# Optimization experiments

Hardware: AMD Instinct MI355X
Metric: run time of the kernel (lower is better)

The kernel has to match this reference:

```python
import jax, jax.numpy as jnp
import numpy as np

T_STEPS = 64   # number of actions (T-1 in the torch code)
BATCH = 512
STATE = 256
ACTION = 64
BELIEF = 1024
HIDDEN = 1024
EMB = 1024
MIN_STD = 0.1


def setup_inputs() -> dict:
    key = jax.random.key(0)
    ks = jax.random.split(key, 16)
    def w(k, shape):
        return jax.random.normal(k, shape, jnp.float32) * 0.02
    return {
        "s_0": jax.random.normal(ks[0], (BATCH, STATE), jnp.float32),
        "A": jax.random.normal(ks[1], (T_STEPS, BATCH, ACTION), jnp.float32),
        "b_0": jax.random.normal(ks[2], (BATCH, BELIEF), jnp.float32),
        "O": jax.random.normal(ks[3], (T_STEPS, BATCH, EMB), jnp.float32),
        "M": jnp.ones((T_STEPS, BATCH, 1), jnp.float32),
        "noise_pri": jax.random.normal(ks[4], (T_STEPS, BATCH, STATE), jnp.float32),
        "noise_pos": jax.random.normal(ks[5], (T_STEPS, BATCH, STATE), jnp.float32),
        # learned parameters (torch nn.Linear convention: y = x @ W.T + b)
        "W_sa": w(ks[6], (BELIEF, STATE + ACTION)), "b_sa": jnp.zeros((BELIEF,), jnp.float32),
        "W_ih": w(ks[7], (3 * BELIEF, BELIEF)), "b_ih": jnp.zeros((3 * BELIEF,), jnp.float32),
        "W_hh": w(ks[8], (3 * BELIEF, BELIEF)), "b_hh": jnp.zeros((3 * BELIEF,), jnp.float32),
        "W_bpri": w(ks[9], (HIDDEN, BELIEF)), "b_bpri": jnp.zeros((HIDDEN,), jnp.float32),
        "W_spri": w(ks[10], (2 * STATE, HIDDEN)), "b_spri": jnp.zeros((2 * STATE,), jnp.float32),
        "W_bpos": w(ks[11], (HIDDEN, BELIEF + EMB)), "b_bpos": jnp.zeros((HIDDEN,), jnp.float32),
        "W_spos": w(ks[12], (2 * STATE, HIDDEN)), "b_spos": jnp.zeros((2 * STATE,), jnp.float32),
    }


def reference(s_0, A, b_0, O, M, noise_pri, noise_pos,
              W_sa, b_sa, W_ih, b_ih, W_hh, b_hh,
              W_bpri, b_bpri, W_spri, b_spri,
              W_bpos, b_bpos, W_spos, b_spos):
    act = jax.nn.relu  # cfg.activation_function = 'relu'

    def gru_cell(x, h):
        # torch GRUCell gate order: r, z, n
        gi = x @ W_ih.T + b_ih      # [B, 3*BELIEF]
        gh = h @ W_hh.T + b_hh
        i_r, i_z, i_n = jnp.split(gi, 3, axis=1)
        h_r, h_z, h_n = jnp.split(gh, 3, axis=1)
        r = jax.nn.sigmoid(i_r + h_r)
        z = jax.nn.sigmoid(i_z + h_z)
        n = jnp.tanh(i_n + r * h_n)
        return (1.0 - z) * n + z * h

    def step(carry, xs):
        b, s = carry  # belief [B,BELIEF], posterior state [B,STATE]
        a_t, o_t, m_t, eps_p, eps_q = xs
        s_in = s * m_t  # non-terminal mask
        x = act(jnp.concatenate([s_in, a_t], axis=1) @ W_sa.T + b_sa)
        b_new = gru_cell(x, b)
        # prior
        pri = act(b_new @ W_bpri.T + b_bpri) @ W_spri.T + b_spri
        mu_p, hp = jnp.split(pri, 2, axis=1)
        std_p = jax.nn.softplus(hp) + MIN_STD
        s_p = mu_p + std_p * eps_p
        # posterior (uses current observation embedding)
        pos = act(jnp.concatenate([b_new, o_t], axis=1) @ W_bpos.T + b_bpos) @ W_spos.T + b_spos
        mu_q, hq = jnp.split(pos, 2, axis=1)
        std_q = jax.nn.softplus(hq) + MIN_STD
        s_q = mu_q + std_q * eps_q
        return (b_new, s_q), (b_new, s_p, mu_p, std_p, s_q, mu_q, std_q)

    (_, _), ys = jax.lax.scan(step, (b_0, s_0), (A, O, M, noise_pri, noise_pos))
    B_out, S_pri, MU_pri, STD_pri, S_pos, MU_pos, STD_pos = ys
    return B_out, S_pri, MU_pri, STD_pri, S_pos, MU_pos, STD_pos
```

## Files before the change

kernel.cpp:

```cpp
#include <hip/hip_runtime.h>
#include <hip/hip_bf16.h>
#include <math.h>

typedef short bf16x8 __attribute__((ext_vector_type(8)));
typedef float f32x4 __attribute__((ext_vector_type(4)));
typedef unsigned short u16;

#define NT 64
#define NB 512
#define NS 256
#define NA 64
#define NBEL 1024

#define OUT_B      0
#define OUT_SPRI   33554432
#define OUT_MUPRI  41943040
#define OUT_STDPRI 50331648
#define OUT_SPOS   58720256
#define OUT_MUPOS  67108864
#define OUT_STDPOS 75497472

__device__ __forceinline__ f32x4 mfma16(bf16x8 a, bf16x8 b, f32x4 c) {
  return __builtin_amdgcn_mfma_f32_16x16x32_bf16(a, b, c, 0, 0, 0);
}

__device__ __forceinline__ u16 f2bf(float f) {
  union { float f; unsigned u; } v; v.f = f;
  return (u16)((v.u + 0x7FFFu + ((v.u >> 16) & 1u)) >> 16);
}

__device__ __forceinline__ bf16x8 ld8bf(const u16* p) { return *(const bf16x8*)p; }

__device__ __forceinline__ bf16x8 cvt8(const float* p) {
  const float4 lo = *(const float4*)p;
  const float4 hi = *(const float4*)(p + 4);
  bf16x8 v;
  v[0] = (short)f2bf(lo.x); v[1] = (short)f2bf(lo.y);
  v[2] = (short)f2bf(lo.z); v[3] = (short)f2bf(lo.w);
  v[4] = (short)f2bf(hi.x); v[5] = (short)f2bf(hi.y);
  v[6] = (short)f2bf(hi.z); v[7] = (short)f2bf(hi.w);
  return v;
}

__device__ __forceinline__ float sigm(float x) { return 1.f / (1.f + __expf(-x)); }
__device__ __forceinline__ float softplus_(float x) {
  if (x > 20.f) return x;
  return log1pf(__expf(x));
}

#define ZACC(acc) { acc[0][0] = (f32x4){0.f,0.f,0.f,0.f}; acc[0][1] = (f32x4){0.f,0.f,0.f,0.f}; \
                    acc[1][0] = (f32x4){0.f,0.f,0.f,0.f}; acc[1][1] = (f32x4){0.f,0.f,0.f,0.f}; }

#define Q4(acc, a0v, a1v, b0v, b1v) \
  acc[0][0] = mfma16(a0v, b0v, acc[0][0]); \
  acc[0][1] = mfma16(a0v, b1v, acc[0][1]); \
  acc[1][0] = mfma16(a1v, b0v, acc[1][0]); \
  acc[1][1] = mfma16(a1v, b1v, acc[1][1]);

__device__ __forceinline__ void red_write(float* L, f32x4 (&acc)[2][2], int l) {
  const int base = l * 16;
#pragma unroll
  for (int i = 0; i < 2; ++i)
#pragma unroll
    for (int j = 0; j < 2; ++j)
#pragma unroll
      for (int q = 0; q < 4; ++q)
        L[base + (i * 2 + j) * 4 + q] = acc[i][j][q];
}
__device__ __forceinline__ void red_add(const float* L, f32x4 (&acc)[2][2], int l) {
  const int base = l * 16;
#pragma unroll
  for (int i = 0; i < 2; ++i)
#pragma unroll
    for (int j = 0; j < 2; ++j)
#pragma unroll
      for (int q = 0; q < 4; ++q)
        acc[i][j][q] += L[base + (i * 2 + j) * 4 + q];
}

__global__ __launch_bounds__(256) void cvt_weights_k(
    const float* __restrict__ wsa, const float* __restrict__ wih,
    const float* __restrict__ whh, const float* __restrict__ wbpri,
    const float* __restrict__ wspri, const float* __restrict__ wbpos,
    const float* __restrict__ wspos, u16* __restrict__ dst) {
  const int S0 = 327680;
  const int S1 = S0 + 3145728;
  const int S2 = S1 + 3145728;
  const int S3 = S2 + 1048576;
  const int S4 = S3 + 524288;
  const int S5 = S4 + 2097152;
  const int S6 = S5 + 524288;
  for (int i = blockIdx.x * blockDim.x + threadIdx.x; i < S6;
       i += gridDim.x * blockDim.x) {
    float v;
    if (i < S0) v = wsa[i];
    else if (i < S1) v = wih[i - S0];
    else if (i < S2) v = whh[i - S1];
    else if (i < S3) v = wbpri[i - S2];
    else if (i < S4) v = wspri[i - S3];
    else if (i < S5) v = wbpos[i - S4];
    else v = wspos[i - S5];
    dst[i] = f2bf(v);
  }
}

__global__ __launch_bounds__(256) void init_carry_k(
    const float* __restrict__ s0, const float* __restrict__ b0,
    const float* __restrict__ Mptr, u16* __restrict__ smask,
    u16* __restrict__ bbf0, float* __restrict__ hf) {
  for (int i = blockIdx.x * blockDim.x + threadIdx.x; i < NB * NBEL;
       i += gridDim.x * blockDim.x) {
    float b = b0[i];
    bbf0[i] = f2bf(b);
    hf[i] = b;
    if (i < NB * NS) {
      int row = i >> 8;
      smask[i] = f2bf(s0[i] * Mptr[row]);
    }
  }
}

__global__ __launch_bounds__(512, 2) void kA(
    const u16* __restrict__ smask, const float* __restrict__ Af,
    const u16* __restrict__ wsa, const float* __restrict__ bsa,
    u16* __restrict__ xbf, const float* __restrict__ Of,
    const u16* __restrict__ wbpos, float* __restrict__ hbO, int t) {
  __shared__ float lred[4][1024];
  const int l = threadIdx.x & 63, r16 = l & 15, kq = l >> 4;
  const int wid8 = threadIdx.x >> 6;
  const int wid = wid8 & 3, kh = wid8 >> 2;
  if (blockIdx.x < 128) {
    const int g = blockIdx.x, bm = g >> 4, bn = g & 15;
    const int row0 = bm * 64 + (wid >> 1) * 32;
    const int col0 = bn * 64 + (wid & 1) * 32;
    f32x4 acc[2][2]; ZACC(acc);
    const u16* A0 = smask + (row0 + r16) * NS + kq * 8;
    const u16* A1 = A0 + 16 * NS;
    const u16* B0 = wsa + (size_t)(col0 + r16) * 320 + kq * 8;
    const u16* B1 = B0 + 16 * 320;
    if (kh == 0) {
#pragma unroll
      for (int k = 0; k < 160; k += 32) {
        bf16x8 a0 = ld8bf(A0 + k), a1 = ld8bf(A1 + k);
        bf16x8 b0 = ld8bf(B0 + k), b1 = ld8bf(B1 + k);
        Q4(acc, a0, a1, b0, b1);
      }
    } else {
#pragma unroll
      for (int k = 160; k < 256; k += 32) {
        bf16x8 a0 = ld8bf(A0 + k), a1 = ld8bf(A1 + k);
        bf16x8 b0 = ld8bf(B0 + k), b1 = ld8bf(B1 + k);
        Q4(acc, a0, a1, b0, b1);
      }
      const float* F0 = Af + (size_t)t * (NB * NA) + (row0 + r16) * NA + kq * 8;
      const float* F1 = F0 + 16 * NA;
      const u16* C0 = wsa + (size_t)(col0 + r16) * 320 + 256 + kq * 8;
      const u16* C1 = C0 + 16 * 320;
#pragma unroll
      for (int k = 0; k < 64; k += 32) {
        bf16x8 a0 = cvt8(F0 + k), a1 = cvt8(F1 + k);
        bf16x8 b0 = ld8bf(C0 + k), b1 = ld8bf(C1 + k);
        Q4(acc, a0, a1, b0, b1);
      }
      red_write(lred[wid], acc, l);
    }
    __syncthreads();
    if (kh == 0) {
      red_add(lred[wid], acc, l);
#pragma unroll
      for (int i = 0; i < 2; ++i)
#pragma unroll
        for (int j = 0; j < 2; ++j)
#pragma unroll
          for (int q = 0; q < 4; ++q) {
            const int row = row0 + i * 16 + kq * 4 + q;
            const int col = col0 + j * 16 + r16;
            xbf[row * NBEL + col] = f2bf(fmaxf(acc[i][j][q] + bsa[col], 0.f));
          }
    }
  } else {
    const int g = blockIdx.x - 128, bm = g >> 4, bn = g & 15;
    const int row0 = bm * 64 + (wid >> 1) * 32;
    const int col0 = bn * 64 + (wid & 1) * 32;
    f32x4 acc[2][2]; ZACC(acc);
    const float* F0 = Of + (size_t)t * (NB * NBEL) + (row0 + r16) * NBEL + kh * 512 + kq * 8;
    const float* F1 = F0 + 16 * NBEL;
    const u16* B0 = wbpos + (size_t)(col0 + r16) * 2048 + 1024 + kh * 512 + kq * 8;
    const u16* B1 = B0 + 16 * 2048;
#pragma unroll 4
    for (int k = 0; k < 512; k += 32) {
      bf16x8 a0 = cvt8(F0 + k), a1 = cvt8(F1 + k);
      bf16x8 b0 = ld8bf(B0 + k), b1 = ld8bf(B1 + k);
      Q4(acc, a0, a1, b0, b1);
    }
    if (kh == 1) red_write(lred[wid], acc, l);
    __syncthreads();
    if (kh == 0) {
      red_add(lred[wid], acc, l);
#pragma unroll
      for (int i = 0; i < 2; ++i)
#pragma unroll
        for (int j = 0; j < 2; ++j)
#pragma unroll
          for (int q = 0; q < 4; ++q) {
            const int row = row0 + i * 16 + kq * 4 + q;
            const int col = col0 + j * 16 + r16;
            hbO[row * NBEL + col] = acc[i][j][q];
          }
    }
  }
}

__global__ __launch_bounds__(512, 2) void kB(
    const u16* __restrict__ xbf, const u16* __restrict__ bprev,
    const u16* __restrict__ wih, const u16* __restrict__ whh,
    const float* __restrict__ bih, const float* __restrict__ bhh,
    float* __restrict__ hf, u16* __restrict__ bcur, float* __restrict__ out,
    const u16* __restrict__ wbpri, const float* __restrict__ bbpri,
    u16* __restrict__ hpri, int t) {
  __shared__ float lred[4][3][1024];
  const int l = threadIdx.x & 63, r16 = l & 15, kq = l >> 4;
  const int wid8 = threadIdx.x >> 6;
  const int wid = wid8 & 3, kh = wid8 >> 2;
  if (blockIdx.x < 128) {
    if (t >= NT) return;
    const int g = blockIdx.x, bm = g >> 4, bn = g & 15;
    const int row0 = bm * 64 + (wid >> 1) * 32;
    const int col0 = bn * 64 + (wid & 1) * 32;
    f32x4 ar[2][2], az[2][2], an[2][2];
    ZACC(ar); ZACC(az); ZACC(an);
    const u16* Asrc = (kh == 0) ? xbf : bprev;
    const u16* W = (kh == 0) ? wih : whh;
    const u16* A0 = Asrc + (row0 + r16) * NBEL + kq * 8;
    const u16* A1 = A0 + 16 * NBEL;
    const u16* Br0 = W + (size_t)(col0 + r16) * NBEL + kq * 8;
    const u16* Br1 = Br0 + 16 * NBEL;
    const u16* Bz0 = W + (size_t)(col0 + 1024 + r16) * NBEL + kq * 8;
    const u16* Bz1 = Bz0 + 16 * NBEL;
    const u16* Bn0 = W + (size_t)(col0 + 2048 + r16) * NBEL + kq * 8;
    const u16* Bn1 = Bn0 + 16 * NBEL;
#pragma unroll 4
    for (int k = 0; k < NBEL; k += 32) {
      bf16x8 a0 = ld8bf(A0 + k), a1 = ld8bf(A1 + k);
      bf16x8 b0 = ld8bf(Br0 + k), b1 = ld8bf(Br1 + k);
      Q4(ar, a0, a1, b0, b1);
      bf16x8 c0 = ld8bf(Bz0 + k), c1 = ld8bf(Bz1 + k);
      Q4(az, a0, a1, c0, c1);
      bf16x8 d0 = ld8bf(Bn0 + k), d1 = ld8bf(Bn1 + k);
      Q4(an, a0, a1, d0, d1);
    }
    if (kh == 1) {
      red_write(lred[wid][0], ar, l);
      red_write(lred[wid][1], az, l);
      red_write(lred[wid][2], an, l);
    }
    __syncthreads();
    if (kh == 0) {
      const int base = l * 16;
#pragma unroll
      for (int i = 0; i < 2; ++i)
#pragma unroll
        for (int j = 0; j < 2; ++j)
#pragma unroll
          for (int q = 0; q < 4; ++q) {
            const int row = row0 + i * 16 + kq * 4 + q;
            const int c = col0 + j * 16 + r16;
            const int li = base + (i * 2 + j) * 4 + q;
            const float r = sigm(ar[i][j][q] + bih[c] + lred[wid][0][li] + bhh[c]);
            const float z = sigm(az[i][j][q] + bih[c + 1024] + lred[wid][1][li] + bhh[c + 1024]);
            const float n = tanhf(an[i][j][q] + bih[c + 2048] +
                                  r * (lred[wid][2][li] + bhh[c + 2048]));
            const float h = hf[row * NBEL + c];
            const float bnew = (1.f - z) * n + z * h;
            hf[row * NBEL + c] = bnew;
            bcur[row * NBEL + c] = f2bf(bnew);
            out[OUT_B + (size_t)t * (NB * NBEL) + row * NBEL + c] = bnew;
          }
    }
  } else {
    if (t < 1) return;
    const int g = blockIdx.x - 128, bm = g >> 4, bn = g & 15;
    const int row0 = bm * 64 + (wid >> 1) * 32;
    const int col0 = bn * 64 + (wid & 1) * 32;
    f32x4 acc[2][2]; ZACC(acc);
    const u16* A0 = bprev + (row0 + r16) * NBEL + kh * 512 + kq * 8;
    const u16* A1 = A0 + 16 * NBEL;
    const u16* B0 = wbpri + (size_t)(col0 + r16) * NBEL + kh * 512 + kq * 8;
    const u16* B1 = B0 + 16 * NBEL;
#pragma unroll 4
    for (int k = 0; k < 512; k += 32) {
      bf16x8 a0 = ld8bf(A0 + k), a1 = ld8bf(A1 + k);
      bf16x8 b0 = ld8bf(B0 + k), b1 = ld8bf(B1 + k);
      Q4(acc, a0, a1, b0, b1);
    }
    if (kh == 1) red_write(lred[wid][0], acc, l);
    __syncthreads();
    if (kh == 0) {
      red_add(lred[wid][0], acc, l);
#pragma unroll
      for (int i = 0; i < 2; ++i)
#pragma unroll
        for (int j = 0; j < 2; ++j)
#pragma unroll
          for (int q = 0; q < 4; ++q) {
            const int row = row0 + i * 16 + kq * 4 + q;
            const int col = col0 + j * 16 + r16;
            hpri[row * NBEL + col] = f2bf(fmaxf(acc[i][j][q] + bbpri[col], 0.f));
          }
    }
  }
}

__global__ __launch_bounds__(512, 2) void kC(
    const u16* __restrict__ bcur, const u16* __restrict__ wbpos,
    const float* __restrict__ bbpos, const float* __restrict__ hbO,
    u16* __restrict__ hbbf,
    const u16* __restrict__ hpri, const u16* __restrict__ wspri,
    const float* __restrict__ bspri, const float* __restrict__ npri,
    float* __restrict__ out, int t) {
  __shared__ float lred[4][2][1024];
  const int l = threadIdx.x & 63, r16 = l & 15, kq = l >> 4;
  const int wid8 = threadIdx.x >> 6;
  const int wid = wid8 & 3, kh = wid8 >> 2;
  if (blockIdx.x < 128) {
    if (t >= NT) return;
    const int g = blockIdx.x, bm = g >> 4, bn = g & 15;
    const int row0 = bm * 64 + (wid >> 1) * 32;
    const int col0 = bn * 64 + (wid & 1) * 32;
    f32x4 acc[2][2]; ZACC(acc);
    const u16* A0 = bcur + (row0 + r16) * NBEL + kh * 512 + kq * 8;
    const u16* A1 = A0 + 16 * NBEL;
    const u16* B0 = wbpos + (size_t)(col0 + r16) * 2048 + kh * 512 + kq * 8;
    const u16* B1 = B0 + 16 * 2048;
#pragma unroll 4
    for (int k = 0; k < 512; k += 32) {
      bf16x8 a0 = ld8bf(A0 + k), a1 = ld8bf(A1 + k);
      bf16x8 b0 = ld8bf(B0 + k), b1 = ld8bf(B1 + k);
      Q4(acc, a0, a1, b0, b1);
    }
    if (kh == 1) red_write(lred[wid][0], acc, l);
    __syncthreads();
    if (kh == 0) {
      red_add(lred[wid][0], acc, l);
#pragma unroll
      for (int i = 0; i < 2; ++i)
#pragma unroll
        for (int j = 0; j < 2; ++j)
#pragma unroll
          for (int q = 0; q < 4; ++q) {
            const int row = row0 + i * 16 + kq * 4 + q;
            const int col = col0 + j * 16 + r16;
            const float v = acc[i][j][q] + hbO[row * NBEL + col] + bbpos[col];
            hbbf[row * NBEL + col] = f2bf(fmaxf(v, 0.f));
          }
    }
  } else {
    if (t < 1) return;
    const int g = blockIdx.x - 128, bm = g >> 2, bn = g & 3;
    const int row0 = bm * 64 + (wid >> 1) * 32;
    const int c0 = bn * 64 + (wid & 1) * 32;
    f32x4 am[2][2], ah[2][2];
    ZACC(am); ZACC(ah);
    const u16* A0 = hpri + (row0 + r16) * NBEL + kh * 512 + kq * 8;
    const u16* A1 = A0 + 16 * NBEL;
    const u16* Bm0 = wspri + (size_t)(c0 + r16) * NBEL + kh * 512 + kq * 8;
    const u16* Bm1 = Bm0 + 16 * NBEL;
    const u16* Bh0 = wspri + (size_t)(c0 + 256 + r16) * NBEL + kh * 512 + kq * 8;
    const u16* Bh1 = Bh0 + 16 * NBEL;
#pragma unroll 4
    for (int k = 0; k < 512; k += 32) {
      bf16x8 a0 = ld8bf(A0 + k), a1 = ld8bf(A1 + k);
      bf16x8 m0 = ld8bf(Bm0 + k), m1 = ld8bf(Bm1 + k);
      Q4(am, a0, a1, m0, m1);
      bf16x8 h0 = ld8bf(Bh0 + k), h1 = ld8bf(Bh1 + k);
      Q4(ah, a0, a1, h0, h1);
    }
    if (kh == 1) {
      red_write(lred[wid][0], am, l);
      red_write(lred[wid][1], ah, l);
    }
    __syncthreads();
    if (kh == 0) {
      red_add(lred[wid][0], am, l);
      red_add(lred[wid][1], ah, l);
      const int tt = t - 1;
#pragma unroll
      for (int i = 0; i < 2; ++i)
#pragma unroll
        for (int j = 0; j < 2; ++j)
#pragma unroll
          for (int q = 0; q < 4; ++q) {
            const int row = row0 + i * 16 + kq * 4 + q;
            const int c = c0 + j * 16 + r16;
            const size_t idx = (size_t)tt * (NB * NS) + row * NS + c;
            const float mu = am[i][j][q] + bspri[c];
            const float hp = ah[i][j][q] + bspri[c + 256];
            const float sd = softplus_(hp) + 0.1f;
            out[OUT_SPRI + idx] = mu + sd * npri[idx];
            out[OUT_MUPRI + idx] = mu;
            out[OUT_STDPRI + idx] = sd;
          }
    }
  }
}

__global__ __launch_bounds__(512, 2) void kD(
    const u16* __restrict__ hbbf, const u16* __restrict__ wspos,
    const float* __restrict__ bspos, const float* __restrict__ npos,
    const float* __restrict__ Mptr, float* __restrict__ out,
    u16* __restrict__ smask, int t) {
  __shared__ float lred[4][2][1024];
  const int l = threadIdx.x & 63, r16 = l & 15, kq = l >> 4;
  const int wid8 = threadIdx.x >> 6;
  const int wid = wid8 & 3, kh = wid8 >> 2;
  const int g = blockIdx.x, bm = g >> 2, bn = g & 3;
  const int row0 = bm * 64 + (wid >> 1) * 32;
  const int c0 = bn * 64 + (wid & 1) * 32;
  f32x4 am[2][2], ah[2][2];
  ZACC(am); ZACC(ah);
  const u16* A0 = hbbf + (row0 + r16) * NBEL + kh * 512 + kq * 8;
  const u16* A1 = A0 + 16 * NBEL;
  const u16* Bm0 = wspos + (size_t)(c0 + r16) * NBEL + kh * 512 + kq * 8;
  const u16* Bm1 = Bm0 + 16 * NBEL;
  const u16* Bh0 = wspos + (size_t)(c0 + 256 + r16) * NBEL + kh * 512 + kq * 8;
  const u16* Bh1 = Bh0 + 16 * NBEL;
#pragma unroll 4
  for (int k = 0; k < 512; k += 32) {
    bf16x8 a0 = ld8bf(A0 + k), a1 = ld8bf(A1 + k);
    bf16x8 m0 = ld8bf(Bm0 + k), m1 = ld8bf(Bm1 + k);
    Q4(am, a0, a1, m0, m1);
    bf16x8 h0 = ld8bf(Bh0 + k), h1 = ld8bf(Bh1 + k);
    Q4(ah, a0, a1, h0, h1);
  }
  if (kh == 1) {
    red_write(lred[wid][0], am, l);
    red_write(lred[wid][1], ah, l);
  }
  __syncthreads();
  if (kh == 0) {
    red_add(lred[wid][0], am, l);
    red_add(lred[wid][1], ah, l);
#pragma unroll
    for (int i = 0; i < 2; ++i)
#pragma unroll
      for (int j = 0; j < 2; ++j)
#pragma unroll
        for (int q = 0; q < 4; ++q) {
          const int row = row0 + i * 16 + kq * 4 + q;
          const int c = c0 + j * 16 + r16;
          const float mu = am[i][j][q] + bspos[c];
          const float hq = ah[i][j][q] + bspos[c + 256];
          const float sd = softplus_(hq) + 0.1f;
          const size_t idx = (size_t)t * (NB * NS) + row * NS + c;
          const float sq = mu + sd * npos[idx];
          out[OUT_SPOS + idx] = sq;
          out[OUT_MUPOS + idx] = mu;
          out[OUT_STDPOS + idx] = sd;
          const float mn = (t < NT - 1) ? Mptr[(t + 1) * NB + row] : 1.f;
          smask[row * NS + c] = f2bf(sq * mn);
        }
  }
}

extern "C" void kernel_launch(void* const* d_in, const int* in_sizes, int n_in,
                              void* d_out, int out_size, void* d_ws, size_t ws_size,
                              hipStream_t stream) {
  const float* s0 = (const float*)d_in[0];
  const float* Af = (const float*)d_in[1];
  const float* b0 = (const float*)d_in[2];
  const float* Of = (const float*)d_in[3];
  const float* Mp = (const float*)d_in[4];
  const float* npri = (const float*)d_in[5];
  const float* npos = (const float*)d_in[6];
  const float* Wsa = (const float*)d_in[7];
  const float* bsa = (const float*)d_in[8];
  const float* Wih = (const float*)d_in[9];
  const float* bih = (const float*)d_in[10];
  const float* Whh = (const float*)d_in[11];
  const float* bhh = (const float*)d_in[12];
  const float* Wbpri = (const float*)d_in[13];
  const float* bbpri = (const float*)d_in[14];
  const float* Wspri = (const float*)d_in[15];
  const float* bspri = (const float*)d_in[16];
  const float* Wbpos = (const float*)d_in[17];
  const float* bbpos = (const float*)d_in[18];
  const float* Wspos = (const float*)d_in[19];
  const float* bspos = (const float*)d_in[20];

  float* out = (float*)d_out;
  char* ws = (char*)d_ws;
  u16* wbase   = (u16*)ws;
  u16* wsa_b   = wbase;
  u16* wih_b   = wbase + 327680;
  u16* whh_b   = wbase + 3473408;
  u16* wbpri_b = wbase + 6619136;
  u16* wspri_b = wbase + 7667712;
  u16* wbpos_b = wbase + 8192000;
  u16* wspos_b = wbase + 10289152;
  u16*   smask = (u16*)  (ws + 21626880);
  u16*   bbf0  = (u16*)  (ws + 21889024);
  u16*   bbf1  = (u16*)  (ws + 22937600);
  float* hf    = (float*)(ws + 23986176);
  u16*   xbf   = (u16*)  (ws + 26083328);
  float* hbO   = (float*)(ws + 27131904);
  u16*   hbbf  = (u16*)  (ws + 29229056);
  u16*   hpri  = (u16*)  (ws + 30277632);

  cvt_weights_k<<<2048, 256, 0, stream>>>(Wsa, Wih, Whh, Wbpri, Wspri, Wbpos,
                                          Wspos, wbase);
  init_carry_k<<<2048, 256, 0, stream>>>(s0, b0, Mp, smask, bbf0, hf);

  for (int t = 0; t < NT; ++t) {
    const u16* bprev = (t & 1) ? bbf1 : bbf0;
    u16* bcur = (t & 1) ? bbf0 : bbf1;
    kA<<<256, 512, 0, stream>>>(smask, Af, wsa_b, bsa, xbf, Of, wbpos_b, hbO, t);
    kB<<<256, 512, 0, stream>>>(xbf, bprev, wih_b, whh_b, bih, bhh, hf, bcur,
                                out, wbpri_b, bbpri, hpri, t);
    kC<<<160, 512, 0, stream>>>(bcur, wbpos_b, bbpos, hbO, hbbf,
                                hpri, wspri_b, bspri, npri, out, t);
    kD<<<32, 512, 0, stream>>>(hbbf, wspos_b, bspos, npos, Mp, out, smask, t);
  }
  {
    const int t = NT;
    const u16* bprev = (t & 1) ? bbf1 : bbf0;
    u16* bcur = (t & 1) ? bbf0 : bbf1;
    kB<<<256, 512, 0, stream>>>(xbf, bprev, wih_b, whh_b, bih, bhh, hf, bcur,
                                out, wbpri_b, bbpri, hpri, t);
    kC<<<160, 512, 0, stream>>>(bcur, wbpos_b, bbpos, hbO, hbbf,
                                hpri, wspri_b, bspri, npri, out, t);
  }
}
```

Before: 10.06 ms.

## Hoist GRU hidden matmul and obs projection into previous step's kernel, fuse x into GRU

Moves the h@W_hh GEMM and the next step's observation projection into the kC kernel, which runs as soon as the new belief exists, so they overlap the prior/posterior head work. The s/a input GEMM is recomputed per block inside the GRU kernel and kept in swizzled LDS, which removes the separate kA launch and the xbf round trip through global memory. This drops one launch per step and shortens the serial chain. In exchange each GRU block does redundant W_sa work, there is an extra fp32 gh buffer, and the kernels are larger with a 128KB LDS footprint.

```diff
diff --git a/kernel.cpp b/kernel.cpp
--- a/kernel.cpp
+++ b/kernel.cpp
@@ -76,6 +76,10 @@
 #pragma unroll
       for (int q = 0; q < 4; ++q)
         acc[i][j][q] += L[base + (i * 2 + j) * 4 + q];
+}
+
+__device__ __forceinline__ int xls_off(int row, int col) {
+  return ((row * NBEL + col) * 2) ^ ((row & 7) << 4);
 }
 
 __global__ __launch_bounds__(256) void cvt_weights_k(
@@ -120,128 +124,162 @@
   }
 }
 
-__global__ __launch_bounds__(512, 2) void kA(
-    const u16* __restrict__ smask, const float* __restrict__ Af,
-    const u16* __restrict__ wsa, const float* __restrict__ bsa,
-    u16* __restrict__ xbf, const float* __restrict__ Of,
-    const u16* __restrict__ wbpos, float* __restrict__ hbO, int t) {
-  __shared__ float lred[4][1024];
+
+__device__ __forceinline__ void dev_gh128(
+    int g, int wid8, int r16, int kq,
+    const u16* __restrict__ bsrc, const u16* __restrict__ whh,
+    const float* __restrict__ bhh, float* __restrict__ gh) {
+  const int bm = g / 24, bn = g % 24;
+  const int row0 = bm * 64 + (wid8 >> 2) * 32;
+  const int col0 = bn * 128 + (wid8 & 3) * 32;
+  f32x4 acc[2][2]; ZACC(acc);
+  const u16* A0 = bsrc + (row0 + r16) * NBEL + kq * 8;
+  const u16* A1 = A0 + 16 * NBEL;
+  const u16* B0 = whh + (size_t)(col0 + r16) * NBEL + kq * 8;
+  const u16* B1 = B0 + 16 * NBEL;
+#pragma unroll 4
+  for (int k = 0; k < NBEL; k += 32) {
+    bf16x8 a0 = ld8bf(A0 + k), a1 = ld8bf(A1 + k);
+    bf16x8 b0 = ld8bf(B0 + k), b1 = ld8bf(B1 + k);
+    Q4(acc, a0, a1, b0, b1);
+  }
+#pragma unroll
+  for (int i = 0; i < 2; ++i)
+#pragma unroll
+    for (int j = 0; j < 2; ++j)
+#pragma unroll
+      for (int q = 0; q < 4; ++q) {
+        const int row = row0 + i * 16 + kq * 4 + q;
+        const int col = col0 + j * 16 + r16;
+        gh[row * 3072 + col] = acc[i][j][q] + bhh[col];
+      }
+}
+
+__device__ __forceinline__ void dev_hbO(
+    int g, int wid, int kh, int r16, int kq, int l, int tt,
+    const float* __restrict__ Of, const u16* __restrict__ wbpos,
+    float* __restrict__ hbO, float* lred) {
+  const int bm = g >> 4, bn = g & 15;
+  const int row0 = bm * 64 + (wid >> 1) * 32;
+  const int col0 = bn * 64 + (wid & 1) * 32;
+  f32x4 acc[2][2]; ZACC(acc);
+  const float* F0 = Of + (size_t)tt * (NB * NBEL) + (row0 + r16) * NBEL + kh * 512 + kq * 8;
+  const float* F1 = F0 + 16 * NBEL;
+  const u16* B0 = wbpos + (size_t)(col0 + r16) * 2048 + 1024 + kh * 512 + kq * 8;
+  const u16* B1 = B0 + 16 * 2048;
+#pragma unroll 4
+  for (int k = 0; k < 512; k += 32) {
+    bf16x8 a0 = cvt8(F0 + k), a1 = cvt8(F1 + k);
+    bf16x8 b0 = ld8bf(B0 + k), b1 = ld8bf(B1 + k);
+    Q4(acc, a0, a1, b0, b1);
+  }
+  if (kh == 1) red_write(lred, acc, l);
+  __syncthreads();
+  if (kh == 0) {
+    red_add(lred, acc, l);
+#pragma unroll
+    for (int i = 0; i < 2; ++i)
+#pragma unroll
+      for (int j = 0; j < 2; ++j)
+#pragma unroll
+        for (int q = 0; q < 4; ++q) {
+          const int row = row0 + i * 16 + kq * 4 + q;
+          const int col = col0 + j * 16 + r16;
+          hbO[row * NBEL + col] = acc[i][j][q];
+        }
+  }
+}
+
+__global__ __launch_bounds__(512, 2) void kPre(
+    const u16* __restrict__ bbf0, const u16* __restrict__ whh,
+    const float* __restrict__ bhh, float* __restrict__ gh,
+    const float* __restrict__ Of, const u16* __restrict__ wbpos,
+    float* __restrict__ hbO0) {
+  __shared__ float lred[4][3][1024];
   const int l = threadIdx.x & 63, r16 = l & 15, kq = l >> 4;
   const int wid8 = threadIdx.x >> 6;
   const int wid = wid8 & 3, kh = wid8 >> 2;
-  if (blockIdx.x < 128) {
-    const int g = blockIdx.x, bm = g >> 4, bn = g & 15;
-    const int row0 = bm * 64 + (wid >> 1) * 32;
-    const int col0 = bn * 64 + (wid & 1) * 32;
-    f32x4 acc[2][2]; ZACC(acc);
-    const u16* A0 = smask + (row0 + r16) * NS + kq * 8;
-    const u16* A1 = A0 + 16 * NS;
-    const u16* B0 = wsa + (size_t)(col0 + r16) * 320 + kq * 8;
-    const u16* B1 = B0 + 16 * 320;
-    if (kh == 0) {
-#pragma unroll
-      for (int k = 0; k < 160; k += 32) {
-        bf16x8 a0 = ld8bf(A0 + k), a1 = ld8bf(A1 + k);
-        bf16x8 b0 = ld8bf(B0 + k), b1 = ld8bf(B1 + k);
-        Q4(acc, a0, a1, b0, b1);
-      }
-    } else {
-#pragma unroll
-      for (int k = 160; k < 256; k += 32) {
-        bf16x8 a0 = ld8bf(A0 + k), a1 = ld8bf(A1 + k);
-        bf16x8 b0 = ld8bf(B0 + k), b1 = ld8bf(B1 + k);
-        Q4(acc, a0, a1, b0, b1);
-      }
-      const float* F0 = Af + (size_t)t * (NB * NA) + (row0 + r16) * NA + kq * 8;
-      const float* F1 = F0 + 16 * NA;
-      const u16* C0 = wsa + (size_t)(col0 + r16) * 320 + 256 + kq * 8;
-      const u16* C1 = C0 + 16 * 320;
-#pragma unroll
-      for (int k = 0; k < 64; k += 32) {
-        bf16x8 a0 = cvt8(F0 + k), a1 = cvt8(F1 + k);
-        bf16x8 b0 = ld8bf(C0 + k), b1 = ld8bf(C1 + k);
-        Q4(acc, a0, a1, b0, b1);
-      }
-      red_write(lred[wid], acc, l);
-    }
-    __syncthreads();
-    if (kh == 0) {
-      red_add(lred[wid], acc, l);
-#pragma unroll
-      for (int i = 0; i < 2; ++i)
-#pragma unroll
-        for (int j = 0; j < 2; ++j)
-#pragma unroll
-          for (int q = 0; q < 4; ++q) {
-            const int row = row0 + i * 16 + kq * 4 + q;
-            const int col = col0 + j * 16 + r16;
-            xbf[row * NBEL + col] = f2bf(fmaxf(acc[i][j][q] + bsa[col], 0.f));
-          }
-    }
+  if (blockIdx.x < 192) {
+    dev_gh128(blockIdx.x, wid8, r16, kq, bbf0, whh, bhh, gh);
   } else {
-    const int g = blockIdx.x - 128, bm = g >> 4, bn = g & 15;
-    const int row0 = bm * 64 + (wid >> 1) * 32;
-    const int col0 = bn * 64 + (wid & 1) * 32;
-    f32x4 acc[2][2]; ZACC(acc);
-    const float* F0 = Of + (size_t)t * (NB * NBEL) + (row0 + r16) * NBEL + kh * 512 + kq * 8;
-    const float* F1 = F0 + 16 * NBEL;
-    const u16* B0 = wbpos + (size_t)(col0 + r16) * 2048 + 1024 + kh * 512 + kq * 8;
-    const u16* B1 = B0 + 16 * 2048;
-#pragma unroll 4
-    for (int k = 0; k < 512; k += 32) {
-      bf16x8 a0 = cvt8(F0 + k), a1 = cvt8(F1 + k);
-      bf16x8 b0 = ld8bf(B0 + k), b1 = ld8bf(B1 + k);
-      Q4(acc, a0, a1, b0, b1);
-    }
-    if (kh == 1) red_write(lred[wid], acc, l);
-    __syncthreads();
-    if (kh == 0) {
-      red_add(lred[wid], acc, l);
-#pragma unroll
-      for (int i = 0; i < 2; ++i)
-#pragma unroll
-        for (int j = 0; j < 2; ++j)
-#pragma unroll
-          for (int q = 0; q < 4; ++q) {
-            const int row = row0 + i * 16 + kq * 4 + q;
-            const int col = col0 + j * 16 + r16;
-            hbO[row * NBEL + col] = acc[i][j][q];
-          }
-    }
-  }
-}
-
-__global__ __launch_bounds__(512, 2) void kB(
-    const u16* __restrict__ xbf, const u16* __restrict__ bprev,
-    const u16* __restrict__ wih, const u16* __restrict__ whh,
-    const float* __restrict__ bih, const float* __restrict__ bhh,
-    float* __restrict__ hf, u16* __restrict__ bcur, float* __restrict__ out,
+    dev_hbO(blockIdx.x - 192, wid, kh, r16, kq, l, 0, Of, wbpos, hbO0,
+            &lred[wid][0][0]);
+  }
+}
+
+__global__ __launch_bounds__(512, 2) void kB2(
+    const u16* __restrict__ smask, const float* __restrict__ Af,
+    const u16* __restrict__ wsa, const float* __restrict__ bsa,
+    const u16* __restrict__ wih, const float* __restrict__ bih,
+    const float* __restrict__ gh, float* __restrict__ hf,
+    const u16* __restrict__ bprev, u16* __restrict__ bcur,
+    float* __restrict__ out,
     const u16* __restrict__ wbpri, const float* __restrict__ bbpri,
     u16* __restrict__ hpri, int t) {
-  __shared__ float lred[4][3][1024];
+  __shared__ __align__(16) char smem[131072];
   const int l = threadIdx.x & 63, r16 = l & 15, kq = l >> 4;
   const int wid8 = threadIdx.x >> 6;
   const int wid = wid8 & 3, kh = wid8 >> 2;
   if (blockIdx.x < 128) {
     if (t >= NT) return;
     const int g = blockIdx.x, bm = g >> 4, bn = g & 15;
-    const int row0 = bm * 64 + (wid >> 1) * 32;
+    for (int task = wid8; task < 16; task += 8) {
+      const int lr0 = (task & 1) * 32;
+      const int c0t = (task >> 1) * 128;
+      const int grow = bm * 64 + lr0;
+      for (int jt = 0; jt < 4; ++jt) {
+        const int col = c0t + jt * 32;
+        f32x4 acc[2][2]; ZACC(acc);
+        const u16* A0 = smask + (grow + r16) * NS + kq * 8;
+        const u16* A1 = A0 + 16 * NS;
+        const u16* B0 = wsa + (size_t)(col + r16) * 320 + kq * 8;
+        const u16* B1 = B0 + 16 * 320;
+#pragma unroll
+        for (int k = 0; k < 256; k += 32) {
+          bf16x8 a0 = ld8bf(A0 + k), a1 = ld8bf(A1 + k);
+          bf16x8 b0 = ld8bf(B0 + k), b1 = ld8bf(B1 + k);
+          Q4(acc, a0, a1, b0, b1);
+        }
+        const float* F0 = Af + (size_t)t * (NB * NA) + (grow + r16) * NA + kq * 8;
+        const float* F1 = F0 + 16 * NA;
+        const u16* C0 = wsa + (size_t)(col + r16) * 320 + 256 + kq * 8;
+        const u16* C1 = C0 + 16 * 320;
+#pragma unroll
+        for (int k = 0; k < 64; k += 32) {
+          bf16x8 a0 = cvt8(F0 + k), a1 = cvt8(F1 + k);
+          bf16x8 b0 = ld8bf(C0 + k), b1 = ld8bf(C1 + k);
+          Q4(acc, a0, a1, b0, b1);
+        }
+#pragma unroll
+        for (int i = 0; i < 2; ++i)
+#pragma unroll
+          for (int j = 0; j < 2; ++j)
+#pragma unroll
+            for (int q = 0; q < 4; ++q) {
+              const int lr = lr0 + i * 16 + kq * 4 + q;
+              const int c = col + j * 16 + r16;
+              const u16 v = f2bf(fmaxf(acc[i][j][q] + bsa[c], 0.f));
+              *(u16*)(smem + xls_off(lr, c)) = v;
+            }
+      }
+    }
+    __syncthreads();
+    const int lrow0 = (wid >> 1) * 32;
+    const int grow0 = bm * 64 + lrow0;
     const int col0 = bn * 64 + (wid & 1) * 32;
     f32x4 ar[2][2], az[2][2], an[2][2];
     ZACC(ar); ZACC(az); ZACC(an);
-    const u16* Asrc = (kh == 0) ? xbf : bprev;
-    const u16* W = (kh == 0) ? wih : whh;
-    const u16* A0 = Asrc + (row0 + r16) * NBEL + kq * 8;
-    const u16* A1 = A0 + 16 * NBEL;
-    const u16* Br0 = W + (size_t)(col0 + r16) * NBEL + kq * 8;
+    const u16* Br0 = wih + (size_t)(col0 + r16) * NBEL + kh * 512 + kq * 8;
     const u16* Br1 = Br0 + 16 * NBEL;
-    const u16* Bz0 = W + (size_t)(col0 + 1024 + r16) * NBEL + kq * 8;
+    const u16* Bz0 = wih + (size_t)(col0 + 1024 + r16) * NBEL + kh * 512 + kq * 8;
     const u16* Bz1 = Bz0 + 16 * NBEL;
-    const u16* Bn0 = W + (size_t)(col0 + 2048 + r16) * NBEL + kq * 8;
+    const u16* Bn0 = wih + (size_t)(col0 + 2048 + r16) * NBEL + kh * 512 + kq * 8;
     const u16* Bn1 = Bn0 + 16 * NBEL;
 #pragma unroll 4
-    for (int k = 0; k < NBEL; k += 32) {
-      bf16x8 a0 = ld8bf(A0 + k), a1 = ld8bf(A1 + k);
+    for (int k = 0; k < 512; k += 32) {
+      const int ks = kh * 512 + k + kq * 8;
+      bf16x8 a0 = *(const bf16x8*)(smem + xls_off(lrow0 + r16, ks));
+      bf16x8 a1 = *(const bf16x8*)(smem + xls_off(lrow0 + 16 + r16, ks));
       bf16x8 b0 = ld8bf(Br0 + k), b1 = ld8bf(Br1 + k);
       Q4(ar, a0, a1, b0, b1);
       bf16x8 c0 = ld8bf(Bz0 + k), c1 = ld8bf(Bz1 + k);
@@ -249,10 +287,12 @@
       bf16x8 d0 = ld8bf(Bn0 + k), d1 = ld8bf(Bn1 + k);
       Q4(an, a0, a1, d0, d1);
     }
+    __syncthreads();
+    float (*lred)[3][1024] = (float (*)[3][1024])smem;
     if (kh == 1) {
-      red_write(lred[wid][0], ar, l);
-      red_write(lred[wid][1], az, l);
-      red_write(lred[wid][2], an, l);
+      red_write(&lred[wid][0][0], ar, l);
+      red_write(&lred[wid][1][0], az, l);
+      red_write(&lred[wid][2][0], an, l);
     }
     __syncthreads();
     if (kh == 0) {
@@ -263,13 +303,14 @@
         for (int j = 0; j < 2; ++j)
 #pragma unroll
           for (int q = 0; q < 4; ++q) {
-            const int row = row0 + i * 16 + kq * 4 + q;
+            const int row = grow0 + i * 16 + kq * 4 + q;
             const int c = col0 + j * 16 + r16;
             const int li = base + (i * 2 + j) * 4 + q;
-            const float r = sigm(ar[i][j][q] + bih[c] + lred[wid][0][li] + bhh[c]);
-            const float z = sigm(az[i][j][q] + bih[c + 1024] + lred[wid][1][li] + bhh[c + 1024]);
-            const float n = tanhf(an[i][j][q] + bih[c + 2048] +
-                                  r * (lred[wid][2][li] + bhh[c + 2048]));
+            const float* ghrow = gh + row * 3072;
+            const float r = sigm(ar[i][j][q] + lred[wid][0][li] + bih[c] + ghrow[c]);
+            const float z = sigm(az[i][j][q] + lred[wid][1][li] + bih[c + 1024] + ghrow[c + 1024]);
+            const float n = tanhf(an[i][j][q] + lred[wid][2][li] + bih[c + 2048] +
+                                  r * ghrow[c + 2048]);
             const float h = hf[row * NBEL + c];
             const float bnew = (1.f - z) * n + z * h;
             hf[row * NBEL + c] = bnew;
@@ -279,6 +320,7 @@
     }
   } else {
     if (t < 1) return;
+    float (*lred)[3][1024] = (float (*)[3][1024])smem;
     const int g = blockIdx.x - 128, bm = g >> 4, bn = g & 15;
     const int row0 = bm * 64 + (wid >> 1) * 32;
     const int col0 = bn * 64 + (wid & 1) * 32;
@@ -293,10 +335,10 @@
       bf16x8 b0 = ld8bf(B0 + k), b1 = ld8bf(B1 + k);
       Q4(acc, a0, a1, b0, b1);
     }
-    if (kh == 1) red_write(lred[wid][0], acc, l);
+    if (kh == 1) red_write(&lred[wid][0][0], acc, l);
     __syncthreads();
     if (kh == 0) {
-      red_add(lred[wid][0], acc, l);
+      red_add(&lred[wid][0][0], acc, l);
 #pragma unroll
       for (int i = 0; i < 2; ++i)
 #pragma unroll
@@ -311,14 +353,17 @@
   }
 }
 
-__global__ __launch_bounds__(512, 2) void kC(
+__global__ __launch_bounds__(512, 2) void kC2(
     const u16* __restrict__ bcur, const u16* __restrict__ wbpos,
-    const float* __restrict__ bbpos, const float* __restrict__ hbO,
+    const float* __restrict__ bbpos, const float* __restrict__ hbOc,
     u16* __restrict__ hbbf,
+    const u16* __restrict__ whh, const float* __restrict__ bhh,
+    float* __restrict__ gh,
+    const float* __restrict__ Of, float* __restrict__ hbOn,
     const u16* __restrict__ hpri, const u16* __restrict__ wspri,
     const float* __restrict__ bspri, const float* __restrict__ npri,
     float* __restrict__ out, int t) {
-  __shared__ float lred[4][2][1024];
+  __shared__ float lred[4][3][1024];
   const int l = threadIdx.x & 63, r16 = l & 15, kq = l >> 4;
   const int wid8 = threadIdx.x >> 6;
   const int wid = wid8 & 3, kh = wid8 >> 2;
@@ -338,10 +383,10 @@
       bf16x8 b0 = ld8bf(B0 + k), b1 = ld8bf(B1 + k);
       Q4(acc, a0, a1, b0, b1);
     }
-    if (kh == 1) red_write(lred[wid][0], acc, l);
+    if (kh == 1) red_write(&lred[wid][0][0], acc, l);
     __syncthreads();
     if (kh == 0) {
-      red_add(lred[wid][0], acc, l);
+      red_add(&lred[wid][0][0], acc, l);
 #pragma unroll
       for (int i = 0; i < 2; ++i)
 #pragma unroll
@@ -350,13 +395,20 @@
           for (int q = 0; q < 4; ++q) {
             const int row = row0 + i * 16 + kq * 4 + q;
             const int col = col0 + j * 16 + r16;
-            const float v = acc[i][j][q] + hbO[row * NBEL + col] + bbpos[col];
+            const float v = acc[i][j][q] + hbOc[row * NBEL + col] + bbpos[col];
             hbbf[row * NBEL + col] = f2bf(fmaxf(v, 0.f));
           }
     }
+  } else if (blockIdx.x < 320) {
+    if (t + 1 >= NT) return;
+    dev_gh128(blockIdx.x - 128, wid8, r16, kq, bcur, whh, bhh, gh);
+  } else if (blockIdx.x < 448) {
+    if (t + 1 >= NT) return;
+    dev_hbO(blockIdx.x - 320, wid, kh, r16, kq, l, t + 1, Of, wbpos, hbOn,
+            &lred[wid][0][0]);
   } else {
     if (t < 1) return;
-    const int g = blockIdx.x - 128, bm = g >> 2, bn = g & 3;
+    const int g = blockIdx.x - 448, bm = g >> 2, bn = g & 3;
     const int row0 = bm * 64 + (wid >> 1) * 32;
     const int c0 = bn * 64 + (wid & 1) * 32;
     f32x4 am[2][2], ah[2][2];
@@ -376,13 +428,13 @@
       Q4(ah, a0, a1, h0, h1);
     }
     if (kh == 1) {
-      red_write(lred[wid][0], am, l);
-      red_write(lred[wid][1], ah, l);
+      red_write(&lred[wid][0][0], am, l);
+      red_write(&lred[wid][1][0], ah, l);
     }
     __syncthreads();
     if (kh == 0) {
-      red_add(lred[wid][0], am, l);
-      red_add(lred[wid][1], ah, l);
+      red_add(&lred[wid][0][0], am, l);
+      red_add(&lred[wid][1][0], ah, l);
       const int tt = t - 1;
 #pragma unroll
       for (int i = 0; i < 2; ++i)
@@ -433,13 +485,13 @@
     Q4(ah, a0, a1, h0, h1);
   }
   if (kh == 1) {
-    red_write(lred[wid][0], am, l);
-    red_write(lred[wid][1], ah, l);
+    red_write(&lred[wid][0][0], am, l);
+    red_write(&lred[wid][1][0], ah, l);
   }
   __syncthreads();
   if (kh == 0) {
-    red_add(lred[wid][0], am, l);
-    red_add(lred[wid][1], ah, l);
+    red_add(&lred[wid][0][0], am, l);
+    red_add(&lred[wid][1][0], ah, l);
 #pragma unroll
     for (int i = 0; i < 2; ++i)
 #pragma unroll
@@ -501,32 +553,39 @@
   u16*   bbf0  = (u16*)  (ws + 21889024);
   u16*   bbf1  = (u16*)  (ws + 22937600);
   float* hf    = (float*)(ws + 23986176);
-  u16*   xbf   = (u16*)  (ws + 26083328);
-  float* hbO   = (float*)(ws + 27131904);
-  u16*   hbbf  = (u16*)  (ws + 29229056);
-  u16*   hpri  = (u16*)  (ws + 30277632);
+  float* gh    = (float*)(ws + 26083328);
+  float* hbO0  = (float*)(ws + 32374784);
+  float* hbO1  = (float*)(ws + 34471936);
+  u16*   hbbf  = (u16*)  (ws + 36569088);
+  u16*   hpri  = (u16*)  (ws + 37617664);
 
   cvt_weights_k<<<2048, 256, 0, stream>>>(Wsa, Wih, Whh, Wbpri, Wspri, Wbpos,
                                           Wspos, wbase);
   init_carry_k<<<2048, 256, 0, stream>>>(s0, b0, Mp, smask, bbf0, hf);
+  kPre<<<320, 512, 0, stream>>>(bbf0, whh_b, bhh, gh, Of, wbpos_b, hbO0);
 
   for (int t = 0; t < NT; ++t) {
     const u16* bprev = (t & 1) ? bbf1 : bbf0;
     u16* bcur = (t & 1) ? bbf0 : bbf1;
-    kA<<<256, 512, 0, stream>>>(smask, Af, wsa_b, bsa, xbf, Of, wbpos_b, hbO, t);
-    kB<<<256, 512, 0, stream>>>(xbf, bprev, wih_b, whh_b, bih, bhh, hf, bcur,
-                                out, wbpri_b, bbpri, hpri, t);
-    kC<<<160, 512, 0, stream>>>(bcur, wbpos_b, bbpos, hbO, hbbf,
-                                hpri, wspri_b, bspri, npri, out, t);
+    float* hbOc = (t & 1) ? hbO1 : hbO0;
+    float* hbOn = (t & 1) ? hbO0 : hbO1;
+    kB2<<<256, 512, 0, stream>>>(smask, Af, wsa_b, bsa, wih_b, bih, gh, hf,
+                                 bprev, bcur, out, wbpri_b, bbpri, hpri, t);
+    kC2<<<480, 512, 0, stream>>>(bcur, wbpos_b, bbpos, hbOc, hbbf,
+                                 whh_b, bhh, gh, Of, hbOn,
+                                 hpri, wspri_b, bspri, npri, out, t);
     kD<<<32, 512, 0, stream>>>(hbbf, wspos_b, bspos, npos, Mp, out, smask, t);
   }
   {
     const int t = NT;
     const u16* bprev = (t & 1) ? bbf1 : bbf0;
     u16* bcur = (t & 1) ? bbf0 : bbf1;
-    kB<<<256, 512, 0, stream>>>(xbf, bprev, wih_b, whh_b, bih, bhh, hf, bcur,
-                                out, wbpri_b, bbpri, hpri, t);
-    kC<<<160, 512, 0, stream>>>(bcur, wbpos_b, bbpos, hbO, hbbf,
-                                hpri, wspri_b, bspri, npri, out, t);
-  }
-}
+    float* hbOc = (t & 1) ? hbO1 : hbO0;
+    float* hbOn = (t & 1) ? hbO0 : hbO1;
+    kB2<<<256, 512, 0, stream>>>(smask, Af, wsa_b, bsa, wih_b, bih, gh, hf,
+                                 bprev, bcur, out, wbpri_b, bbpri, hpri, t);
+    kC2<<<480, 512, 0, stream>>>(bcur, wbpos_b, bbpos, hbOc, hbbf,
+                                 whh_b, bhh, gh, Of, hbOn,
+                                 hpri, wspri_b, bspri, npri, out, t);
+  }
+}
```

Result: slower. 13.70 ms (+36.2%).
